# Kernel optimization log

Measured on AMD Instinct MI355X. Metric: run time of the kernel, lower is better.

The kernel has to match this reference:

```python
import jax, jax.numpy as jnp
import numpy as np

VOCAB = 50257
INPUT_DIM = 1024
CUTOFF_ENDS = [0, 10000, 30000, VOCAB]
PROJ_DIMS = [1024, 512, 256]  # input_dim // factor**i, factor=2.0
N_TOKENS = 8192


def setup_inputs() -> dict:
    key = jax.random.key(0)
    ks = jax.random.split(key, 16)
    inp = {
        "x": jax.random.normal(ks[0], (N_TOKENS, INPUT_DIM), dtype=jnp.float32),
        "target": jax.random.randint(ks[1], (N_TOKENS,), 0, VOCAB, dtype=jnp.int64),
    }
    # Per-cluster projection weights (nn.Linear(input_dim, proj_dim, bias=False) -> [proj_dim, input_dim])
    # and output layers (nn.Linear(proj_dim, cluster_size) -> weight [cluster, proj_dim], bias [cluster]).
    for i in range(3):
        cluster = CUTOFF_ENDS[i + 1] - CUTOFF_ENDS[i]
        pd = PROJ_DIMS[i]
        inp[f"p{i}"] = jax.random.normal(ks[2 + 3 * i], (pd, INPUT_DIM), dtype=jnp.float32) * 0.02
        inp[f"w{i}"] = jax.random.normal(ks[3 + 3 * i], (cluster, pd), dtype=jnp.float32) * 0.02
        inp[f"b{i}"] = jnp.zeros((cluster,), dtype=jnp.float32)
    return inp


def reference(x, target, p0, w0, b0, p1, w1, b1, p2, w2, b2):
    # Faithful to torch AdaptiveSoftmax.forward(input, target):
    # per-cluster: gather tokens whose target falls in [l, r), project, classify,
    # cross-entropy. Clusters partition [0, vocab), so every token hits exactly
    # one cluster; we compute each cluster's pipeline densely over all tokens
    # (jit-friendly, no data-dependent shapes) and select per-token via the mask.
    projs, ws, bs = [p0, p1, p2], [w0, w1, w2], [b0, b1, b2]
    target = target.astype(jnp.int32)
    nll = jnp.zeros((x.shape[0],), dtype=x.dtype)
    for i in range(3):
        l, r = CUTOFF_ENDS[i], CUTOFF_ENDS[i + 1]
        mask = (target >= l) & (target < r)
        hidden = jnp.einsum('nd,pd->np', x, projs[i])          # [N, proj_dim]
        logits = jnp.einsum('np,cp->nc', hidden, ws[i]) + bs[i]  # [N, cluster]
        logp = jax.nn.log_softmax(logits, axis=-1)
        t_i = jnp.clip(target - l, 0, r - l - 1)
        nll_i = -jnp.take_along_axis(logp, t_i[:, None], axis=1)[:, 0]
        nll = jnp.where(mask, nll_i, nll)
    loss = nll.sum()  # == sum of per-cluster reduction='sum' cross-entropies
    return loss, nll
```

## Files before the change

### kernel.cpp

```cpp
#include <hip/hip_runtime.h>
#include <cmath>

#define N_TOK 8192
#define DIM 1024

using bf16x8 = __attribute__((ext_vector_type(8))) short;
using f32x4  = __attribute__((ext_vector_type(4))) float;

__device__ __forceinline__ unsigned f2bf(float f) {
  unsigned u = __float_as_uint(f);
  return (u + 0x7fffu + ((u >> 16) & 1u)) >> 16;
}

__device__ __forceinline__ void gll16(const void* g, void* l) {
  __builtin_amdgcn_global_load_lds(
      (const __attribute__((address_space(1))) void*)g,
      (__attribute__((address_space(3))) void*)l, 16, 0, 0);
}

__global__ __launch_bounds__(1024) void k_setup(const int* __restrict__ tgt,
                                                int* __restrict__ cnt,
                                                int* __restrict__ hoff,
                                                int* __restrict__ perm) {
  __shared__ int base[3];
  int t = threadIdx.x;
  if (t < 3) base[t] = 0;
  __syncthreads();
  for (int i = t; i < N_TOK; i += 1024) {
    int tg = tgt[i];
    int cid = (tg < 10000) ? 0 : (tg < 30000 ? 1 : 2);
    int slot = atomicAdd(&base[cid], 1);
    perm[cid * N_TOK + slot] = i;
  }
  __syncthreads();
  if (t < 3) cnt[t] = base[t];
  if (t == 0) {
    hoff[0] = 0;
    hoff[1] = base[0] * 1024;
    hoff[2] = base[0] * 1024 + base[1] * 512;
  }
}

__global__ __launch_bounds__(256) void k_hc(
    const float* __restrict__ x,
    const float* __restrict__ p0, const float* __restrict__ p1, const float* __restrict__ p2,
    const float* __restrict__ w0, const float* __restrict__ w1, const float* __restrict__ w2,
    const int* __restrict__ perm, const int* __restrict__ cnt, const int* __restrict__ hoffs,
    unsigned short* __restrict__ wb, unsigned short* __restrict__ hb) {
  if (blockIdx.z == 0) {
    const int nw0 = 10240000, nw1 = 10240000, nw2 = 5185792;
    const int total4 = (nw0 + nw1 + nw2) >> 2;
    for (int i = blockIdx.x * 256 + threadIdx.x; i < total4; i += 512 * 256) {
      int e = i << 2;
      const float* src;
      if (e < nw0) src = w0 + e;
      else if (e < nw0 + nw1) src = w1 + (e - nw0);
      else src = w2 + (e - nw0 - nw1);
      float4 v = *(const float4*)src;
      uint2 o;
      o.x = f2bf(v.x) | (f2bf(v.y) << 16);
      o.y = f2bf(v.z) | (f2bf(v.w) << 16);
      *(uint2*)(wb + e) = o;
    }
    return;
  }
  const int cid = blockIdx.z - 1;
  const int pd = (cid == 0) ? 1024 : (cid == 1) ? 512 : 256;
  const int count = cnt[cid];
  if (count == 0) return;
  const int nchd = pd >> 7;
  const int chunk = blockIdx.x % nchd;
  const int tile = blockIdx.x / nchd;
  if (tile * 128 >= count) return;
  const int dim0 = chunk * 128, row0 = tile * 128;
  const float* P = (cid == 0) ? p0 : (cid == 1) ? p1 : p2;
  const size_t hoff = (size_t)hoffs[cid];

  __shared__ char pool[34816];
  __shared__ int ptoks[128];
  short* stg = (short*)pool;
  short* Os = (short*)pool;

  const int t = threadIdx.x, wv = t >> 6, lane = t & 63, m = lane & 15, q = lane >> 4;
  const int wr = wv >> 1, wc = wv & 1;

  if (t < 128) {
    int idx = row0 + t;
    ptoks[t] = perm[cid * N_TOK + min(idx, count - 1)];
  }
  __syncthreads();

  const int s0 = t, s1 = t + 256;
  const int r0 = s0 >> 2, g0 = (s0 & 3) ^ ((r0 >> 1) & 3);
  const int r1 = s1 >> 2, g1 = (s1 & 3) ^ ((r1 >> 1) & 3);
  const uint4* srcA0 = (const uint4*)(x + (size_t)ptoks[r0] * DIM) + g0 * 2;
  const uint4* srcA1 = (const uint4*)(x + (size_t)ptoks[r1] * DIM) + g1 * 2;
  const uint4* srcB0 = (const uint4*)(P + (size_t)(dim0 + r0) * DIM) + g0 * 2;
  const uint4* srcB1 = (const uint4*)(P + (size_t)(dim0 + r1) * DIM) + g1 * 2;

  f32x4 acc[4][4];
  #pragma unroll
  for (int rt = 0; rt < 4; ++rt)
    #pragma unroll
    for (int ct = 0; ct < 4; ++ct) acc[rt][ct] = (f32x4){0.f, 0.f, 0.f, 0.f};

  const int sR = (q ^ ((m >> 1) & 3)) * 8;

  {
    uint4 a0 = srcA0[0], a1 = srcA0[1], a2 = srcA1[0], a3 = srcA1[1];
    uint4 b0 = srcB0[0], b1 = srcB0[1], b2 = srcB1[0], b3 = srcB1[1];
    uint4 o;
    o.x = (a0.x >> 16) | (a0.y & 0xFFFF0000u); o.y = (a0.z >> 16) | (a0.w & 0xFFFF0000u);
    o.z = (a1.x >> 16) | (a1.y & 0xFFFF0000u); o.w = (a1.z >> 16) | (a1.w & 0xFFFF0000u);
    *(uint4*)&stg[s0 * 8] = o;
    o.x = (a2.x >> 16) | (a2.y & 0xFFFF0000u); o.y = (a2.z >> 16) | (a2.w & 0xFFFF0000u);
    o.z = (a3.x >> 16) | (a3.y & 0xFFFF0000u); o.w = (a3.z >> 16) | (a3.w & 0xFFFF0000u);
    *(uint4*)&stg[s1 * 8] = o;
    o.x = (b0.x >> 16) | (b0.y & 0xFFFF0000u); o.y = (b0.z >> 16) | (b0.w & 0xFFFF0000u);
    o.z = (b1.x >> 16) | (b1.y & 0xFFFF0000u); o.w = (b1.z >> 16) | (b1.w & 0xFFFF0000u);
    *(uint4*)&stg[4096 + s0 * 8] = o;
    o.x = (b2.x >> 16) | (b2.y & 0xFFFF0000u); o.y = (b2.z >> 16) | (b2.w & 0xFFFF0000u);
    o.z = (b3.x >> 16) | (b3.y & 0xFFFF0000u); o.w = (b3.z >> 16) | (b3.w & 0xFFFF0000u);
    *(uint4*)&stg[4096 + s1 * 8] = o;
  }

  int p = 0;
  for (int ks = 0; ks < 32; ++ks) {
    __syncthreads();
    const bool nxt = (ks + 1) < 32;
    uint4 a0, a1, a2, a3, b0, b1, b2, b3;
    if (nxt) {
      int ko = (ks + 1) * 8;
      a0 = srcA0[ko]; a1 = srcA0[ko + 1]; a2 = srcA1[ko]; a3 = srcA1[ko + 1];
      b0 = srcB0[ko]; b1 = srcB0[ko + 1]; b2 = srcB1[ko]; b3 = srcB1[ko + 1];
    }
    short* SAp = stg + p * 8192;
    short* SBp = SAp + 4096;
    bf16x8 af[4];
    #pragma unroll
    for (int rt = 0; rt < 4; ++rt)
      af[rt] = *(bf16x8*)&SAp[(wr * 64 + rt * 16 + m) * 32 + sR];
    #pragma unroll
    for (int ct = 0; ct < 4; ++ct) {
      bf16x8 bb = *(bf16x8*)&SBp[(wc * 64 + ct * 16 + m) * 32 + sR];
      #pragma unroll
      for (int rt = 0; rt < 4; ++rt)
        acc[rt][ct] = __builtin_amdgcn_mfma_f32_16x16x32_bf16(af[rt], bb, acc[rt][ct], 0, 0, 0);
    }
    if (nxt) {
      short* DA = stg + (p ^ 1) * 8192;
      short* DB = DA + 4096;
      uint4 o;
      o.x = (a0.x >> 16) | (a0.y & 0xFFFF0000u); o.y = (a0.z >> 16) | (a0.w & 0xFFFF0000u);
      o.z = (a1.x >> 16) | (a1.y & 0xFFFF0000u); o.w = (a1.z >> 16) | (a1.w & 0xFFFF0000u);
      *(uint4*)&DA[s0 * 8] = o;
      o.x = (a2.x >> 16) | (a2.y & 0xFFFF0000u); o.y = (a2.z >> 16) | (a2.w & 0xFFFF0000u);
      o.z = (a3.x >> 16) | (a3.y & 0xFFFF0000u); o.w = (a3.z >> 16) | (a3.w & 0xFFFF0000u);
      *(uint4*)&DA[s1 * 8] = o;
      o.x = (b0.x >> 16) | (b0.y & 0xFFFF0000u); o.y = (b0.z >> 16) | (b0.w & 0xFFFF0000u);
      o.z = (b1.x >> 16) | (b1.y & 0xFFFF0000u); o.w = (b1.z >> 16) | (b1.w & 0xFFFF0000u);
      *(uint4*)&DB[s0 * 8] = o;
      o.x = (b2.x >> 16) | (b2.y & 0xFFFF0000u); o.y = (b2.z >> 16) | (b2.w & 0xFFFF0000u);
      o.z = (b3.x >> 16) | (b3.y & 0xFFFF0000u); o.w = (b3.z >> 16) | (b3.w & 0xFFFF0000u);
      *(uint4*)&DB[s1 * 8] = o;
    }
    p ^= 1;
  }

  __syncthreads();
  #pragma unroll
  for (int rt = 0; rt < 4; ++rt)
    #pragma unroll
    for (int ct = 0; ct < 4; ++ct)
      #pragma unroll
      for (int rr = 0; rr < 4; ++rr)
        Os[(wr * 64 + rt * 16 + q * 4 + rr) * 136 + wc * 64 + ct * 16 + m] =
            (short)f2bf(acc[rt][ct][rr]);
  __syncthreads();
  {
    int orow = t >> 1, oh = t & 1;
    int slot = row0 + orow;
    if (slot < count) {
      unsigned short* dst = hb + hoff + (size_t)slot * pd + dim0 + oh * 64;
      const short* src = &Os[orow * 136 + oh * 64];
      #pragma unroll
      for (int i = 0; i < 8; ++i)
        *(uint4*)(dst + i * 8) = *(const uint4*)(src + i * 8);
    }
  }
}

__global__ __launch_bounds__(256) void k_lse(
    const unsigned short* __restrict__ hb, const unsigned short* __restrict__ wb,
    const float* __restrict__ b0_, const float* __restrict__ b1_, const float* __restrict__ b2_,
    const int* __restrict__ tgt, const int* __restrict__ perm,
    const int* __restrict__ cnt, const int* __restrict__ hoffs,
    float* __restrict__ psum, float* __restrict__ tlog) {
  const int cid = blockIdx.z;
  const int pd     = (cid == 0) ? 1024  : (cid == 1) ? 512   : 256;
  const int cstart = (cid == 0) ? 0     : (cid == 1) ? 10000 : 30000;
  const int csize  = (cid == 0) ? 10000 : (cid == 1) ? 20000 : 20257;
  const size_t woff = (cid == 0) ? 0 : (cid == 1) ? (size_t)10240000 : (size_t)20480000;
  const float* bias = (cid == 0) ? b0_ : (cid == 1) ? b1_ : b2_;
  const int count = cnt[cid];
  if (count == 0) return;
  const unsigned ntile = (unsigned)(count + 127) >> 7;
  const int nchunk = (csize + 127) >> 7;
  const int cpx = (nchunk + 7) >> 3;

  const unsigned d = blockIdx.x;
  const int x8 = d & 7;
  const unsigned g = d >> 3;
  const unsigned ci = g / ntile;
  if (ci >= (unsigned)cpx) return;
  const int chunk = x8 * cpx + (int)ci;
  if (chunk >= nchunk) return;
  const int tile = (int)(g - ci * ntile);
  const int col0 = chunk * 128, row0 = tile * 128;
  const size_t hoff = (size_t)hoffs[cid];

  __shared__ short SA[2][4096];
  __shared__ short SB[2][4096];
  __shared__ int ptoks[128];
  __shared__ int tlocs[128];

  const int t = threadIdx.x, wv = t >> 6, lane = t & 63, m = lane & 15, q = lane >> 4;
  const int wr = wv >> 1, wc = wv & 1;

  if (t < 128) {
    int idx = row0 + t;
    int tok = perm[cid * N_TOK + min(idx, count - 1)];
    ptoks[t] = tok;
    tlocs[t] = tgt[tok] - cstart;
  }

  const int sub = lane >> 2;
  const int gsw = (lane & 3) ^ ((sub >> 1) & 3);
  const unsigned short *pA[2], *pB[2];
  short *lA[2][2], *lB[2][2];
  #pragma unroll
  for (int i = 0; i < 2; ++i) {
    int ia = wv * 2 + i;
    int ra = ia * 16 + sub;
    pA[i] = hb + hoff + (size_t)min(row0 + ra, count - 1) * pd + gsw * 8;
    pB[i] = wb + woff + (size_t)min(col0 + ra, csize - 1) * pd + gsw * 8;
    #pragma unroll
    for (int pp = 0; pp < 2; ++pp) {
      lA[i][pp] = &SA[pp][ia * 512];
      lB[i][pp] = &SB[pp][ia * 512];
    }
  }

  float bc[4];
  #pragma unroll
  for (int ct = 0; ct < 4; ++ct)
    bc[ct] = bias[min(col0 + wc * 64 + ct * 16 + m, csize - 1)];

  f32x4 acc[4][4];
  #pragma unroll
  for (int rt = 0; rt < 4; ++rt)
    #pragma unroll
    for (int ct = 0; ct < 4; ++ct) acc[rt][ct] = (f32x4){0.f, 0.f, 0.f, 0.f};

  const int sR = (q ^ ((m >> 1) & 3)) * 8;
  const int nk = pd >> 5;

  #pragma unroll
  for (int i = 0; i < 2; ++i) { gll16(pA[i], lA[i][0]); gll16(pB[i], lB[i][0]); }

  int p = 0;
  for (int ks = 0; ks < nk; ++ks) {
    __syncthreads();
    if (ks + 1 < nk) {
      int ko = (ks + 1) * 32;
      #pragma unroll
      for (int i = 0; i < 2; ++i) {
        gll16(pA[i] + ko, lA[i][p ^ 1]);
        gll16(pB[i] + ko, lB[i][p ^ 1]);
      }
    }
    bf16x8 af[4];
    #pragma unroll
    for (int rt = 0; rt < 4; ++rt)
      af[rt] = *(bf16x8*)&SA[p][(wr * 64 + rt * 16 + m) * 32 + sR];
    #pragma unroll
    for (int ct = 0; ct < 4; ++ct) {
      bf16x8 bb = *(bf16x8*)&SB[p][(wc * 64 + ct * 16 + m) * 32 + sR];
      #pragma unroll
      for (int rt = 0; rt < 4; ++rt)
        acc[rt][ct] = __builtin_amdgcn_mfma_f32_16x16x32_bf16(af[rt], bb, acc[rt][ct], 0, 0, 0);
    }
    p ^= 1;
  }

  float run[4][4] = {{0.f}}, tcap[4][4] = {{0.f}};
  int tfnd[4][4] = {{0}};
  int tl[4][4];
  #pragma unroll
  for (int rt = 0; rt < 4; ++rt)
    #pragma unroll
    for (int rr = 0; rr < 4; ++rr)
      tl[rt][rr] = tlocs[wr * 64 + rt * 16 + q * 4 + rr];

  #pragma unroll
  for (int ct = 0; ct < 4; ++ct) {
    int colg = col0 + wc * 64 + ct * 16 + m;
    bool cok = colg < csize;
    #pragma unroll
    for (int rt = 0; rt < 4; ++rt)
      #pragma unroll
      for (int rr = 0; rr < 4; ++rr) {
        float val = acc[rt][ct][rr] + bc[ct];
        if (cok) {
          run[rt][rr] += __expf(val);
          if (tl[rt][rr] == colg) { tcap[rt][rr] = val; tfnd[rt][rr] = 1; }
        }
      }
  }

  #pragma unroll
  for (int rt = 0; rt < 4; ++rt)
    #pragma unroll
    for (int rr = 0; rr < 4; ++rr) {
      float v = run[rt][rr];
      v += __shfl_xor(v, 1, 64);
      v += __shfl_xor(v, 2, 64);
      v += __shfl_xor(v, 4, 64);
      v += __shfl_xor(v, 8, 64);
      int rowl = wr * 64 + rt * 16 + q * 4 + rr;
      if (row0 + rowl < count) {
        int tok = ptoks[rowl];
        if (m == 0) atomicAdd(&psum[tok], v);
        if (tfnd[rt][rr]) tlog[tok] = tcap[rt][rr];
      }
    }
}

__global__ __launch_bounds__(1024) void k_final(const float* __restrict__ psum,
                                                const float* __restrict__ tlog,
                                                float* __restrict__ out) {
  __shared__ float part[16];
  int t = threadIdx.x;
  float s = 0.f;
  for (int n = t; n < N_TOK; n += 1024) {
    float v = __logf(psum[n]) - tlog[n];
    out[1 + n] = v;
    s += v;
  }
  #pragma unroll
  for (int off = 32; off > 0; off >>= 1) s += __shfl_down(s, off, 64);
  if ((t & 63) == 0) part[t >> 6] = s;
  __syncthreads();
  if (t < 64) {
    float v = (t < 16) ? part[t] : 0.f;
    #pragma unroll
    for (int off = 8; off > 0; off >>= 1) v += __shfl_down(v, off, 64);
    if (t == 0) out[0] = v;
  }
}

extern "C" void kernel_launch(void* const* d_in, const int* in_sizes, int n_in,
                              void* d_out, int out_size, void* d_ws, size_t ws_size,
                              hipStream_t stream) {
  const float* x  = (const float*)d_in[0];
  const int* tgt  = (const int*)d_in[1];
  const float* p0 = (const float*)d_in[2];
  const float* w0 = (const float*)d_in[3];
  const float* b0 = (const float*)d_in[4];
  const float* p1 = (const float*)d_in[5];
  const float* w1 = (const float*)d_in[6];
  const float* b1 = (const float*)d_in[7];
  const float* p2 = (const float*)d_in[8];
  const float* w2 = (const float*)d_in[9];
  const float* b2 = (const float*)d_in[10];
  float* out = (float*)d_out;

  char* ws = (char*)d_ws;
  int* cnt            = (int*)(ws + 0);
  int* hoff           = (int*)(ws + 64);
  int* perm           = (int*)(ws + 256);
  unsigned short* wb  = (unsigned short*)(ws + 131072);
  unsigned short* hb  = (unsigned short*)(ws + 51462656);
  float* psum         = (float*)(ws + 68239872);
  float* tlog         = (float*)(ws + 68272640);

  hipMemsetAsync(psum, 0, N_TOK * sizeof(float), stream);
  k_setup<<<dim3(1), dim3(1024), 0, stream>>>(tgt, cnt, hoff, perm);
  k_hc<<<dim3(512, 1, 4), dim3(256), 0, stream>>>(x, p0, p1, p2, w0, w1, w2,
                                                  perm, cnt, hoff, wb, hb);
  k_lse<<<dim3(10240, 1, 3), dim3(256), 0, stream>>>(hb, wb, b0, b1, b2, tgt, perm, cnt, hoff,
                                                     psum, tlog);
  k_final<<<dim3(1), dim3(1024), 0, stream>>>(psum, tlog, out);
}
```

Baseline: 504.1 us.

## Triple-buffer LDS tiles with explicit vmcnt waits in the logits GEMM

Replaces the double-buffered global_load_lds pipeline with a three-stage ring buffer that prefetches two k-steps ahead. Each iteration waits only on the oldest loads via s_waitcnt vmcnt and a raw s_barrier instead of draining every load through __syncthreads. MFMA sections also raise wave priority with s_setprio. The goal is to hide global memory latency better. The cost is 50% more LDS, which may reduce occupancy, and correctness now relies on hand-counted vmcnt values.

```diff
diff --git a/kernel.cpp b/kernel.cpp
--- a/kernel.cpp
+++ b/kernel.cpp
@@ -219,8 +219,8 @@
   const int col0 = chunk * 128, row0 = tile * 128;
   const size_t hoff = (size_t)hoffs[cid];
 
-  __shared__ short SA[2][4096];
-  __shared__ short SB[2][4096];
+  __shared__ short SA[3 * 4096];
+  __shared__ short SB[3 * 4096];
   __shared__ int ptoks[128];
   __shared__ int tlocs[128];
 
@@ -233,22 +233,20 @@
     ptoks[t] = tok;
     tlocs[t] = tgt[tok] - cstart;
   }
+  __syncthreads();
 
   const int sub = lane >> 2;
   const int gsw = (lane & 3) ^ ((sub >> 1) & 3);
   const unsigned short *pA[2], *pB[2];
-  short *lA[2][2], *lB[2][2];
+  short *lA[2], *lB[2];
   #pragma unroll
   for (int i = 0; i < 2; ++i) {
     int ia = wv * 2 + i;
     int ra = ia * 16 + sub;
     pA[i] = hb + hoff + (size_t)min(row0 + ra, count - 1) * pd + gsw * 8;
     pB[i] = wb + woff + (size_t)min(col0 + ra, csize - 1) * pd + gsw * 8;
-    #pragma unroll
-    for (int pp = 0; pp < 2; ++pp) {
-      lA[i][pp] = &SA[pp][ia * 512];
-      lB[i][pp] = &SB[pp][ia * 512];
-    }
+    lA[i] = &SA[ia * 512];
+    lB[i] = &SB[ia * 512];
   }
 
   float bc[4];
@@ -266,32 +264,43 @@
   const int nk = pd >> 5;
 
   #pragma unroll
-  for (int i = 0; i < 2; ++i) { gll16(pA[i], lA[i][0]); gll16(pB[i], lB[i][0]); }
+  for (int i = 0; i < 2; ++i) { gll16(pA[i], lA[i]); gll16(pB[i], lB[i]); }
+  #pragma unroll
+  for (int i = 0; i < 2; ++i) { gll16(pA[i] + 32, lA[i] + 4096); gll16(pB[i] + 32, lB[i] + 4096); }
 
   int p = 0;
   for (int ks = 0; ks < nk; ++ks) {
-    __syncthreads();
-    if (ks + 1 < nk) {
-      int ko = (ks + 1) * 32;
+    if (ks + 1 < nk) asm volatile("s_waitcnt vmcnt(4)" ::: "memory");
+    else             asm volatile("s_waitcnt vmcnt(0)" ::: "memory");
+    __builtin_amdgcn_s_barrier();
+    asm volatile("" ::: "memory");
+    if (ks + 2 < nk) {
+      const int ko = (ks + 2) * 32;
+      const int pn = (p == 0) ? 2 : p - 1;
+      const int lo = pn * 4096;
       #pragma unroll
       for (int i = 0; i < 2; ++i) {
-        gll16(pA[i] + ko, lA[i][p ^ 1]);
-        gll16(pB[i] + ko, lB[i][p ^ 1]);
+        gll16(pA[i] + ko, lA[i] + lo);
+        gll16(pB[i] + ko, lB[i] + lo);
       }
     }
+    const int pb = p * 4096;
     bf16x8 af[4];
     #pragma unroll
     for (int rt = 0; rt < 4; ++rt)
-      af[rt] = *(bf16x8*)&SA[p][(wr * 64 + rt * 16 + m) * 32 + sR];
+      af[rt] = *(bf16x8*)&SA[pb + (wr * 64 + rt * 16 + m) * 32 + sR];
+    __builtin_amdgcn_s_setprio(1);
     #pragma unroll
     for (int ct = 0; ct < 4; ++ct) {
-      bf16x8 bb = *(bf16x8*)&SB[p][(wc * 64 + ct * 16 + m) * 32 + sR];
+      bf16x8 bb = *(bf16x8*)&SB[pb + (wc * 64 + ct * 16 + m) * 32 + sR];
       #pragma unroll
       for (int rt = 0; rt < 4; ++rt)
         acc[rt][ct] = __builtin_amdgcn_mfma_f32_16x16x32_bf16(af[rt], bb, acc[rt][ct], 0, 0, 0);
     }
-    p ^= 1;
-  }
+    __builtin_amdgcn_s_setprio(0);
+    p = (p == 2) ? 0 : p + 1;
+  }
+  asm volatile("" ::: "memory");
 
   float run[4][4] = {{0.f}}, tcap[4][4] = {{0.f}};
   int tfnd[4][4] = {{0}};
```

After: 522.3 us. 1.04x slower.
